# Kernel tuning notes

Measured on AMD Instinct MI355X. Metric: run time of the kernel, lower is better.

## Reference

```python
import jax, jax.numpy as jnp
import numpy as np

B, CD, NF, V, D = 16384, 13, 26, 100000, 64
BOT = [256, 128]
TOP = [512, 256, 128]
NUM_EMB = NF + 1            # 27 (bottom output + 26 categorical)
NUM_INTER = NUM_EMB * (NUM_EMB - 1) // 2  # 351
TOP_IN = NUM_INTER + NUM_EMB * D          # 2079
BN_INV = 1.0 / np.sqrt(1.0 + 1e-5)        # eval-mode BatchNorm: running_mean=0, running_var=1


def _lin(key, fan_in, fan_out):
    kw, kb = jax.random.split(key)
    s = 1.0 / np.sqrt(fan_in)
    W = jax.random.uniform(kw, (fan_in, fan_out), minval=-s, maxval=s, dtype=jnp.float32)
    b = jax.random.uniform(kb, (fan_out,), minval=-s, maxval=s, dtype=jnp.float32)
    return W, b


def setup_inputs() -> dict:
    key = jax.random.key(0)
    ks = jax.random.split(key, 16)
    continuous = jax.random.normal(ks[0], (B, CD), dtype=jnp.float32)
    cat_idx = jax.random.randint(ks[1], (B, NF), 0, V, dtype=jnp.int32)
    emb_tables = jax.random.normal(ks[2], (NF, V, D), dtype=jnp.float32)  # nn.Embedding init ~ N(0,1)
    W1, b1 = _lin(ks[3], CD, BOT[0]);   g1 = jnp.ones((BOT[0],)); be1 = jnp.zeros((BOT[0],))
    W2, b2 = _lin(ks[4], BOT[0], BOT[1]); g2 = jnp.ones((BOT[1],)); be2 = jnp.zeros((BOT[1],))
    W3, b3 = _lin(ks[5], BOT[1], D)
    W4, b4 = _lin(ks[6], TOP_IN, TOP[0]); g4 = jnp.ones((TOP[0],)); be4 = jnp.zeros((TOP[0],))
    W5, b5 = _lin(ks[7], TOP[0], TOP[1]); g5 = jnp.ones((TOP[1],)); be5 = jnp.zeros((TOP[1],))
    W6, b6 = _lin(ks[8], TOP[1], TOP[2]); g6 = jnp.ones((TOP[2],)); be6 = jnp.zeros((TOP[2],))
    W7, b7 = _lin(ks[9], TOP[2], 1)
    return dict(continuous=continuous, cat_idx=cat_idx, emb_tables=emb_tables,
                W1=W1, b1=b1, g1=g1, be1=be1, W2=W2, b2=b2, g2=g2, be2=be2, W3=W3, b3=b3,
                W4=W4, b4=b4, g4=g4, be4=be4, W5=W5, b5=b5, g5=g5, be5=be5,
                W6=W6, b6=b6, g6=g6, be6=be6, W7=W7, b7=b7)


def _bn(x, g, b):
    # eval-mode BatchNorm1d with running_mean=0, running_var=1
    return g * (x * BN_INV) + b


def reference(continuous, cat_idx, emb_tables,
              W1, b1, g1, be1, W2, b2, g2, be2, W3, b3,
              W4, b4, g4, be4, W5, b5, g5, be5, W6, b6, g6, be6, W7, b7):
    # Bottom MLP: 13 -> 256 -> 128 -> 64
    h = jax.nn.relu(_bn(continuous @ W1 + b1, g1, be1))
    h = jax.nn.relu(_bn(h @ W2 + b2, g2, be2))
    bottom = h @ W3 + b3                         # [B, D]

    # Embedding gather: one table per categorical feature
    emb = emb_tables[jnp.arange(NF), cat_idx]    # [B, NF, D]
    all_emb = jnp.concatenate([bottom[:, None, :], emb], axis=1)  # [B, 27, D]

    # Pairwise dot-product interactions via one bmm + triu gather
    Z = jnp.einsum('bnd,bmd->bnm', all_emb, all_emb)              # [B, 27, 27]
    iu, ju = np.triu_indices(NUM_EMB, k=1)                        # row-major i<j (matches torch loop order)
    inter = Z[:, iu, ju]                                          # [B, 351]

    top_in = jnp.concatenate([inter, all_emb.reshape(all_emb.shape[0], -1)], axis=1)  # [B, 2079]

    # Top MLP: 2079 -> 512 -> 256 -> 128 -> 1
    t = jax.nn.relu(_bn(top_in @ W4 + b4, g4, be4))
    t = jax.nn.relu(_bn(t @ W5 + b5, g5, be5))
    t = jax.nn.relu(_bn(t @ W6 + b6, g6, be6))
    scores = t @ W7 + b7                                          # [B, 1]
    return scores
```

## Files before the change

kernel.cpp:

```cpp
#include <hip/hip_runtime.h>
#include <stdint.h>
#include <stddef.h>

#define BATCH   16384
#define CDIM    13
#define NFEAT   26
#define VROWS   100000
#define EDIM    64
#define NEMB    27
#define NINTER  351
#define TOPIN   2079
#define KP4     2112
#define BN_INVF 0.9999950000374997f

typedef __attribute__((ext_vector_type(8)))  __bf16 bf16x8;
typedef __attribute__((ext_vector_type(4)))  float  f32x4;
typedef __attribute__((ext_vector_type(16))) float  f32x16;
typedef __attribute__((ext_vector_type(4)))  uint32_t uint4v;

__device__ __forceinline__ uint32_t f2bf(float f){
  uint32_t u = __float_as_uint(f);
  return (u + 0x7fffu + ((u >> 16) & 1u)) >> 16;
}
__device__ __forceinline__ float bf2f(uint32_t h){ return __uint_as_float(h << 16); }
__device__ __forceinline__ uint32_t pack2(float a, float b){
  return f2bf(a) | (f2bf(b) << 16);
}
__device__ __forceinline__ void async_load16(const void* g, void* l){
  __builtin_amdgcn_global_load_lds(
      (const __attribute__((address_space(1))) uint32_t*)g,
      (__attribute__((address_space(3))) uint32_t*)l, 16, 0, 0);
}
__device__ __forceinline__ int rswz(int row){ return ((row ^ (row >> 3)) & 7) << 3; }

__device__ __forceinline__ void transpose_tile(
    float (*tile)[65], const float* __restrict__ src, unsigned short* __restrict__ dst,
    int K, int N, int Kpad, int remap, int kb, int nb){
  int k0 = kb*64, n0 = nb*64, t = threadIdx.x;
  int srcBase = remap ? ((k0 < 1728) ? (k0 + 351) : (k0 - 1728)) : k0;
  #pragma unroll 4
  for(int p = 0; p < 16; p++){
    int kr = p*4 + (t >> 6), nc = t & 63;
    float v = 0.f;
    if(k0 + kr < K && (n0 + nc) < N) v = src[(size_t)(srcBase + kr) * N + n0 + nc];
    tile[kr][nc] = v;
  }
  __syncthreads();
  #pragma unroll 4
  for(int p = 0; p < 16; p++){
    int nr = p*4 + (t >> 6), kc = t & 63;
    if(k0 + kc < Kpad && (n0 + nr) < N)
      dst[(size_t)(n0 + nr) * Kpad + k0 + kc] = (unsigned short)f2bf(tile[kc][nr]);
  }
}

__global__ __launch_bounds__(256) void prep(
    const float* __restrict__ cont,
    const float* __restrict__ W1, const float* __restrict__ W2, const float* __restrict__ W3,
    const float* __restrict__ W4, const float* __restrict__ W5, const float* __restrict__ W6,
    unsigned short* __restrict__ xphi, unsigned short* __restrict__ xplo,
    unsigned short* __restrict__ W1t, unsigned short* __restrict__ W2t,
    unsigned short* __restrict__ W3t, unsigned short* __restrict__ W4t,
    unsigned short* __restrict__ W5t, unsigned short* __restrict__ W6t){
  __shared__ float tile[64][65];
  int bid = blockIdx.x;
  if(bid < 264){ transpose_tile(tile, W4, W4t, TOPIN, 512, KP4, 1, bid % 33, bid / 33); }
  else if(bid < 296){ int r = bid-264; transpose_tile(tile, W5, W5t, 512, 256, 512, 0, r % 8, r / 8); }
  else if(bid < 304){ int r = bid-296; transpose_tile(tile, W6, W6t, 256, 128, 256, 0, r % 4, r / 4); }
  else if(bid < 312){ int r = bid-304; transpose_tile(tile, W2, W2t, 256, 128, 256, 0, r % 4, r / 4); }
  else if(bid < 314){ int r = bid-312; transpose_tile(tile, W3, W3t, 128, 64, 128, 0, r, 0); }
  else if(bid < 318){ int r = bid-314; transpose_tile(tile, W1, W1t, CDIM, 256, 32, 0, 0, r); }
  else {
    int row = (bid - 318) * 256 + threadIdx.x;
    const float* xr = cont + (size_t)row * CDIM;
    uint32_t uh[16], ul[16];
    #pragma unroll
    for(int k = 0; k < 16; k++){
      uint32_t h0=0, h1=0, l0=0, l1=0;
      if(2*k < CDIM){
        float x = xr[2*k]; h0 = f2bf(x); l0 = f2bf(x - bf2f(h0));
      }
      if(2*k+1 < CDIM){
        float x = xr[2*k+1]; h1 = f2bf(x); l1 = f2bf(x - bf2f(h1));
      }
      uh[k] = h0 | (h1 << 16);
      ul[k] = l0 | (l1 << 16);
    }
    #pragma unroll
    for(int s = 0; s < 4; s++){
      uint4v vh, vl;
      #pragma unroll
      for(int e = 0; e < 4; e++){ vh[e] = uh[4*s+e]; vl[e] = ul[4*s+e]; }
      *(uint4v*)(xphi + (size_t)row*32 + s*8) = vh;
      *(uint4v*)(xplo + (size_t)row*32 + s*8) = vl;
    }
  }
}

__global__ __launch_bounds__(256) void bottom_mfma(
    const unsigned short* __restrict__ xphi, const unsigned short* __restrict__ xplo,
    const unsigned short* __restrict__ W1t, const unsigned short* __restrict__ W2t,
    const unsigned short* __restrict__ W3t,
    const float* __restrict__ b1, const float* __restrict__ g1, const float* __restrict__ be1,
    const float* __restrict__ b2, const float* __restrict__ g2, const float* __restrict__ be2,
    const float* __restrict__ b3,
    unsigned short* __restrict__ bottomBF){
  __shared__ unsigned short h1hi[64*256];
  __shared__ unsigned short h1lo[64*256];
  __shared__ unsigned short h2hi[64*128];
  __shared__ unsigned short h2lo[64*128];
  int t = threadIdx.x, w = t >> 6, l = t & 63;
  int m0 = blockIdx.x * 64;
  int lr = l & 15, lk = (l >> 4) * 8;

  {
    bf16x8 axh[4], axl[4];
    #pragma unroll
    for(int mt = 0; mt < 4; mt++){
      size_t ro = (size_t)(m0 + mt*16 + lr) * 32 + lk;
      axh[mt] = *(const bf16x8*)(xphi + ro);
      axl[mt] = *(const bf16x8*)(xplo + ro);
    }
    #pragma unroll
    for(int nt = 0; nt < 4; nt++){
      int n = (w*4 + nt)*16 + lr;
      bf16x8 bw = *(const bf16x8*)(W1t + (size_t)n*32 + lk);
      f32x4 acc[4];
      #pragma unroll
      for(int mt = 0; mt < 4; mt++){
        #pragma unroll
        for(int e = 0; e < 4; e++) acc[mt][e] = 0.f;
        acc[mt] = __builtin_amdgcn_mfma_f32_16x16x32_bf16(axh[mt], bw, acc[mt], 0, 0, 0);
        acc[mt] = __builtin_amdgcn_mfma_f32_16x16x32_bf16(axl[mt], bw, acc[mt], 0, 0, 0);
      }
      float sc = g1[n]*BN_INVF, bo = be1[n], bi = b1[n];
      #pragma unroll
      for(int mt = 0; mt < 4; mt++){
        #pragma unroll
        for(int q = 0; q < 4; q++){
          int row = mt*16 + (l >> 4)*4 + q;
          float y = fmaxf(sc*(acc[mt][q] + bi) + bo, 0.f);
          uint32_t hb = f2bf(y);
          int idx = row*256 + (n ^ rswz(row));
          h1hi[idx] = (unsigned short)hb;
          h1lo[idx] = (unsigned short)f2bf(y - bf2f(hb));
        }
      }
    }
  }
  __syncthreads();

  {
    f32x4 acc[4][2];
    #pragma unroll
    for(int mt = 0; mt < 4; mt++)
      #pragma unroll
      for(int nt = 0; nt < 2; nt++)
        #pragma unroll
        for(int e = 0; e < 4; e++) acc[mt][nt][e] = 0.f;
    for(int ks = 0; ks < 8; ks++){
      bf16x8 bw[2];
      #pragma unroll
      for(int nt = 0; nt < 2; nt++){
        int n = (w*2 + nt)*16 + lr;
        bw[nt] = *(const bf16x8*)(W2t + (size_t)n*256 + ks*32 + lk);
      }
      #pragma unroll
      for(int mt = 0; mt < 4; mt++){
        int row = mt*16 + lr;
        int idx = row*256 + ((ks*32 + lk) ^ rswz(row));
        bf16x8 ah = *(const bf16x8*)(h1hi + idx);
        bf16x8 al = *(const bf16x8*)(h1lo + idx);
        #pragma unroll
        for(int nt = 0; nt < 2; nt++){
          acc[mt][nt] = __builtin_amdgcn_mfma_f32_16x16x32_bf16(ah, bw[nt], acc[mt][nt], 0, 0, 0);
          acc[mt][nt] = __builtin_amdgcn_mfma_f32_16x16x32_bf16(al, bw[nt], acc[mt][nt], 0, 0, 0);
        }
      }
    }
    #pragma unroll
    for(int nt = 0; nt < 2; nt++){
      int n = (w*2 + nt)*16 + lr;
      float sc = g2[n]*BN_INVF, bo = be2[n], bi = b2[n];
      #pragma unroll
      for(int mt = 0; mt < 4; mt++){
        #pragma unroll
        for(int q = 0; q < 4; q++){
          int row = mt*16 + (l >> 4)*4 + q;
          float y = fmaxf(sc*(acc[mt][nt][q] + bi) + bo, 0.f);
          uint32_t hb = f2bf(y);
          int idx = row*128 + (n ^ rswz(row));
          h2hi[idx] = (unsigned short)hb;
          h2lo[idx] = (unsigned short)f2bf(y - bf2f(hb));
        }
      }
    }
  }
  __syncthreads();

  {
    f32x4 acc[4];
    #pragma unroll
    for(int mt = 0; mt < 4; mt++)
      #pragma unroll
      for(int e = 0; e < 4; e++) acc[mt][e] = 0.f;
    int n = w*16 + lr;
    for(int ks = 0; ks < 4; ks++){
      bf16x8 bw = *(const bf16x8*)(W3t + (size_t)n*128 + ks*32 + lk);
      #pragma unroll
      for(int mt = 0; mt < 4; mt++){
        int row = mt*16 + lr;
        int idx = row*128 + ((ks*32 + lk) ^ rswz(row));
        bf16x8 ah = *(const bf16x8*)(h2hi + idx);
        bf16x8 al = *(const bf16x8*)(h2lo + idx);
        acc[mt] = __builtin_amdgcn_mfma_f32_16x16x32_bf16(ah, bw, acc[mt], 0, 0, 0);
        acc[mt] = __builtin_amdgcn_mfma_f32_16x16x32_bf16(al, bw, acc[mt], 0, 0, 0);
      }
    }
    float bi = b3[n];
    #pragma unroll
    for(int mt = 0; mt < 4; mt++){
      #pragma unroll
      for(int q = 0; q < 4; q++){
        int row = m0 + mt*16 + (l >> 4)*4 + q;
        bottomBF[(size_t)row*64 + n] = (unsigned short)f2bf(acc[mt][q] + bi);
      }
    }
  }
}

__global__ __launch_bounds__(256) void interact(
    const unsigned short* __restrict__ bottomBF, const int* __restrict__ cat_idx,
    const float* __restrict__ emb, unsigned short* __restrict__ top_in){
  __shared__ unsigned short inter_s[4][352];
  int w = threadIdx.x >> 6, l = threadIdx.x & 63;
  int b = blockIdx.x * 4 + w;
  int r = l & 31, h = l >> 5;
  bool active = (r < NEMB);
  uint4v q[4];
  if(active && r == 0){
    const unsigned short* sb = bottomBF + (size_t)b * 64;
    #pragma unroll
    for(int s = 0; s < 4; s++) q[s] = *(const uint4v*)(sb + h*8 + s*16);
  } else if(active){
    int f = r - 1;
    int idx = cat_idx[b * NFEAT + f];
    const float* src = emb + ((size_t)f * VROWS + (size_t)idx) * 64;
    #pragma unroll
    for(int s = 0; s < 4; s++){
      int k0 = h*8 + s*16;
      float4 v0 = *(const float4*)(src + k0);
      float4 v1 = *(const float4*)(src + k0 + 4);
      q[s][0] = pack2(v0.x, v0.y); q[s][1] = pack2(v0.z, v0.w);
      q[s][2] = pack2(v1.x, v1.y); q[s][3] = pack2(v1.z, v1.w);
    }
  } else {
    #pragma unroll
    for(int s = 0; s < 4; s++){ q[s][0]=0; q[s][1]=0; q[s][2]=0; q[s][3]=0; }
  }
  if(active){
    #pragma unroll
    for(int s = 0; s < 4; s++)
      *(uint4v*)(top_in + (size_t)b*KP4 + r*64 + h*8 + s*16) = q[s];
  }
  f32x16 acc;
  #pragma unroll
  for(int i = 0; i < 16; i++) acc[i] = 0.f;
  #pragma unroll
  for(int s = 0; s < 4; s++){
    bf16x8 a = __builtin_bit_cast(bf16x8, q[s]);
    acc = __builtin_amdgcn_mfma_f32_32x32x16_bf16(a, a, acc, 0, 0, 0);
  }
  if(active){
    #pragma unroll
    for(int qq = 0; qq < 16; qq++){
      int i = (qq & 3) + 8*(qq >> 2) + 4*h;
      if(i < r){
        int p = i*(53 - i)/2 + (r - i - 1);
        inter_s[w][p] = (unsigned short)f2bf(acc[qq]);
      }
    }
  }
  __syncthreads();
  size_t basei = (size_t)b*KP4 + 1728;
  for(int t0 = l; t0 < 176; t0 += 64){
    uint32_t lo = inter_s[w][2*t0];
    uint32_t hi = (2*t0 + 1 < NINTER) ? (uint32_t)inter_s[w][2*t0 + 1] : 0u;
    *(uint32_t*)(top_in + basei + 2*t0) = lo | (hi << 16);
  }
  if(l < 16) *(uint32_t*)(top_in + (size_t)b*KP4 + 2080 + 2*l) = 0;
}

template<int KSTEPS, int NB>
__global__ __launch_bounds__(512, 2) void gemm_deep(
    const unsigned short* __restrict__ A, int sA,
    const unsigned short* __restrict__ Bw, int sB,
    const float* __restrict__ bias, const float* __restrict__ gg,
    const float* __restrict__ be,
    unsigned short* __restrict__ out, int sOut){
  __shared__ char smem[3*49152];
  int nwg = gridDim.x;
  int bid = blockIdx.x;
  int lin = (bid & 7) * (nwg >> 3) + (bid >> 3);
  int m0 = (lin / NB) * 256, n0 = (lin % NB) * 128;
  int t = threadIdx.x, w = t >> 6, l = t & 63;
  int wr = (w >> 1) * 64, wc = (w & 1) * 64;
  f32x4 acc[4][4];
  #pragma unroll
  for(int i = 0; i < 4; i++)
    #pragma unroll
    for(int j = 0; j < 4; j++)
      #pragma unroll
      for(int e = 0; e < 4; e++) acc[i][j][e] = 0.f;

  const unsigned short* g[6];
  int ldsOff[6];
  #pragma unroll
  for(int i = 0; i < 6; i++){
    if(i < 4){
      int o = i*8192 + t*16;
      int row = o >> 7;
      int cb  = (o & 127) ^ ((row & 7) << 4);
      g[i] = A + (size_t)(m0 + row)*sA + (cb >> 1);
      ldsOff[i] = o;
    } else {
      int o = (i-4)*8192 + t*16;
      int row = o >> 7;
      int cb  = (o & 127) ^ ((row & 7) << 4);
      g[i] = Bw + (size_t)(n0 + row)*sB + (cb >> 1);
      ldsOff[i] = 32768 + o;
    }
  }
  int lr = l & 15;
  int o1 = ((l >> 4) * 16) ^ ((l & 7) << 4);

  #pragma unroll
  for(int i = 0; i < 6; i++) async_load16(g[i], smem + ldsOff[i]);
  #pragma unroll
  for(int i = 0; i < 6; i++) async_load16(g[i] + 64, smem + 49152 + ldsOff[i]);
  asm volatile("s_waitcnt vmcnt(6)" ::: "memory");
  __builtin_amdgcn_s_barrier();

  for(int kt = 0; kt < KSTEPS; kt++){
    int cur = kt % 3;
    int nxt2 = (kt + 2) % 3;
    int ksrc = (kt + 2 < KSTEPS) ? (kt + 2) : (KSTEPS - 1);
    const char* bA = smem + cur*49152;
    const char* bB = bA + 32768;
    #pragma unroll
    for(int i = 0; i < 3; i++)
      async_load16(g[i] + ksrc*64, smem + nxt2*49152 + ldsOff[i]);
    {
      bf16x8 af[4], bfr[4];
      #pragma unroll
      for(int x = 0; x < 4; x++){
        af[x]  = *(const bf16x8*)(bA + (wr + x*16 + lr)*128 + o1);
        bfr[x] = *(const bf16x8*)(bB + (wc + x*16 + lr)*128 + o1);
      }
      __builtin_amdgcn_s_barrier();
      __builtin_amdgcn_s_setprio(1);
      #pragma unroll
      for(int tr = 0; tr < 4; tr++)
        #pragma unroll
        for(int tc = 0; tc < 4; tc++)
          acc[tr][tc] = __builtin_amdgcn_mfma_f32_16x16x32_bf16(af[tr], bfr[tc], acc[tr][tc], 0, 0, 0);
      __builtin_amdgcn_s_setprio(0);
    }
    __builtin_amdgcn_s_barrier();
    #pragma unroll
    for(int i = 3; i < 6; i++)
      async_load16(g[i] + ksrc*64, smem + nxt2*49152 + ldsOff[i]);
    {
      bf16x8 af[4], bfr[4];
      int ko = o1 ^ 64;
      #pragma unroll
      for(int x = 0; x < 4; x++){
        af[x]  = *(const bf16x8*)(bA + (wr + x*16 + lr)*128 + ko);
        bfr[x] = *(const bf16x8*)(bB + (wc + x*16 + lr)*128 + ko);
      }
      asm volatile("s_waitcnt vmcnt(6)" ::: "memory");
      __builtin_amdgcn_s_barrier();
      __builtin_amdgcn_s_setprio(1);
      #pragma unroll
      for(int tr = 0; tr < 4; tr++)
        #pragma unroll
        for(int tc = 0; tc < 4; tc++)
          acc[tr][tc] = __builtin_amdgcn_mfma_f32_16x16x32_bf16(af[tr], bfr[tc], acc[tr][tc], 0, 0, 0);
      __builtin_amdgcn_s_setprio(0);
    }
    __builtin_amdgcn_s_barrier();
  }

  #pragma unroll
  for(int tc = 0; tc < 4; tc++){
    int n = n0 + wc + tc*16 + lr;
    float sc = gg[n]*BN_INVF, bo = be[n], bi = bias[n];
    #pragma unroll
    for(int tr = 0; tr < 4; tr++){
      int mb = m0 + wr + tr*16 + (l >> 4)*4;
      #pragma unroll
      for(int qq = 0; qq < 4; qq++){
        float y = fmaxf(sc*(acc[tr][tc][qq] + bi) + bo, 0.f);
        out[(size_t)(mb + qq)*sOut + n] = (unsigned short)f2bf(y);
      }
    }
  }
}

__global__ __launch_bounds__(256) void gemm_tail(
    const unsigned short* __restrict__ h4,
    const unsigned short* __restrict__ W5t,
    const float* __restrict__ b5, const float* __restrict__ g5, const float* __restrict__ be5,
    const unsigned short* __restrict__ W6t,
    const float* __restrict__ b6, const float* __restrict__ g6, const float* __restrict__ be6,
    const float* __restrict__ W7, const float* __restrict__ b7,
    float* __restrict__ scores){
  __shared__ char smem[74752];
  unsigned short* h5 = (unsigned short*)(smem + 40960);
  float* pscore = (float*)(smem + 73728);
  int t = threadIdx.x, w = t >> 6, l = t & 63;
  int m0 = blockIdx.x * 64;
  int lr = l & 15;
  int o1 = ((l >> 4) * 16) ^ ((l & 7) << 4);

  f32x4 acc5[4][4];
  #pragma unroll
  for(int i = 0; i < 4; i++)
    #pragma unroll
    for(int j = 0; j < 4; j++)
      #pragma unroll
      for(int e = 0; e < 4; e++) acc5[i][j][e] = 0.f;

  const unsigned short* gA[2]; int ldsA[2];
  #pragma unroll
  for(int i = 0; i < 2; i++){
    int o = i*4096 + t*16;
    int row = o >> 7;
    int cb = (o & 127) ^ ((row & 7) << 4);
    gA[i] = h4 + (size_t)(m0 + row)*512 + (cb >> 1);
    ldsA[i] = o;
  }
  const unsigned short* gB[8]; int ldsB[8];
  #pragma unroll
  for(int i = 0; i < 8; i++){
    int o = i*4096 + t*16;
    int row = o >> 7;
    int cb = (o & 127) ^ ((row & 7) << 4);
    gB[i] = W5t + (size_t)row*512 + (cb >> 1);
    ldsB[i] = 8192 + o;
  }

  for(int kt = 0; kt < 8; kt++){
    #pragma unroll
    for(int i = 0; i < 2; i++) async_load16(gA[i] + kt*64, smem + ldsA[i]);
    #pragma unroll
    for(int i = 0; i < 8; i++) async_load16(gB[i] + kt*64, smem + ldsB[i]);
    __syncthreads();
    #pragma unroll
    for(int ks = 0; ks < 2; ks++){
      int ko = o1 ^ (ks << 6);
      bf16x8 af[4], bfr[4];
      #pragma unroll
      for(int x = 0; x < 4; x++){
        af[x]  = *(const bf16x8*)(smem + (x*16 + lr)*128 + ko);
        bfr[x] = *(const bf16x8*)(smem + 8192 + (w*64 + x*16 + lr)*128 + ko);
      }
      #pragma unroll
      for(int tr = 0; tr < 4; tr++)
        #pragma unroll
        for(int tc = 0; tc < 4; tc++)
          acc5[tr][tc] = __builtin_amdgcn_mfma_f32_16x16x32_bf16(af[tr], bfr[tc], acc5[tr][tc], 0, 0, 0);
    }
    __syncthreads();
  }

  #pragma unroll
  for(int i = 0; i < 8; i++){
    int o = i*4096 + t*16;
    int row = o >> 8;
    int cb = (o & 255) ^ ((row & 15) << 4);
    async_load16(W6t + (size_t)row*256 + (cb >> 1), smem + o);
  }
  #pragma unroll
  for(int tc = 0; tc < 4; tc++){
    int c = w*64 + tc*16 + lr;
    float sc = g5[c]*BN_INVF, bo = be5[c], bi = b5[c];
    #pragma unroll
    for(int tr = 0; tr < 4; tr++){
      #pragma unroll
      for(int qq = 0; qq < 4; qq++){
        int row = tr*16 + (l >> 4)*4 + qq;
        float y = fmaxf(sc*(acc5[tr][tc][qq] + bi) + bo, 0.f);
        h5[row*256 + (c ^ rswz(row))] = (unsigned short)f2bf(y);
      }
    }
  }
  __syncthreads();

  f32x4 acc6[4][2];
  #pragma unroll
  for(int i = 0; i < 4; i++)
    #pragma unroll
    for(int j = 0; j < 2; j++)
      #pragma unroll
      for(int e = 0; e < 4; e++) acc6[i][j][e] = 0.f;
  int lk = (l >> 4) * 8;
  int lk2 = (l >> 4) * 16;
  #pragma unroll
  for(int half = 0; half < 2; half++){
    if(half == 1){
      __syncthreads();
      #pragma unroll
      for(int i = 0; i < 8; i++){
        int o = i*4096 + t*16;
        int row = o >> 8;
        int cb = (o & 255) ^ ((row & 15) << 4);
        async_load16(W6t + (size_t)row*256 + 128 + (cb >> 1), smem + o);
      }
      __syncthreads();
    }
    #pragma unroll
    for(int ks = 0; ks < 4; ks++){
      bf16x8 af6[4], bfr6[2];
      #pragma unroll
      for(int mt = 0; mt < 4; mt++){
        int row = mt*16 + lr;
        af6[mt] = *(const bf16x8*)(h5 + row*256 + ((half*128 + ks*32 + lk) ^ rswz(row)));
      }
      #pragma unroll
      for(int nt = 0; nt < 2; nt++){
        int row = w*32 + nt*16 + lr;
        bfr6[nt] = *(const bf16x8*)(smem + row*256 + ((ks*64 + lk2) ^ (lr << 4)));
      }
      #pragma unroll
      for(int mt = 0; mt < 4; mt++)
        #pragma unroll
        for(int nt = 0; nt < 2; nt++)
          acc6[mt][nt] = __builtin_amdgcn_mfma_f32_16x16x32_bf16(af6[mt], bfr6[nt], acc6[mt][nt], 0, 0, 0);
    }
  }

  float pr[16];
  #pragma unroll
  for(int nt = 0; nt < 2; nt++){
    int c = w*32 + nt*16 + lr;
    float sc = g6[c]*BN_INVF, bo = be6[c], bi = b6[c];
    float w7c = W7[c];
    #pragma unroll
    for(int mt = 0; mt < 4; mt++){
      #pragma unroll
      for(int qq = 0; qq < 4; qq++){
        float v = fmaxf(sc*(acc6[mt][nt][qq] + bi) + bo, 0.f) * w7c;
        if(nt == 0) pr[mt*4 + qq] = v; else pr[mt*4 + qq] += v;
      }
    }
  }
  #pragma unroll
  for(int mask = 1; mask < 16; mask <<= 1){
    #pragma unroll
    for(int i = 0; i < 16; i++) pr[i] += __shfl_xor(pr[i], mask, 64);
  }
  if(lr == 0){
    #pragma unroll
    for(int mt = 0; mt < 4; mt++)
      #pragma unroll
      for(int qq = 0; qq < 4; qq++)
        pscore[w*64 + mt*16 + (l >> 4)*4 + qq] = pr[mt*4 + qq];
  }
  __syncthreads();
  if(t < 64){
    float s = b7[0] + pscore[t] + pscore[64 + t] + pscore[128 + t] + pscore[192 + t];
    scores[m0 + t] = s;
  }
}

static inline size_t alignup(size_t x){ return (x + 255) & ~(size_t)255; }

extern "C" void kernel_launch(void* const* d_in, const int* in_sizes, int n_in,
                              void* d_out, int out_size, void* d_ws, size_t ws_size,
                              hipStream_t stream){
  const float* cont = (const float*)d_in[0];
  const int*   cat  = (const int*)  d_in[1];
  const float* emb  = (const float*)d_in[2];
  const float* W1 = (const float*)d_in[3],  *b1 = (const float*)d_in[4];
  const float* g1 = (const float*)d_in[5],  *be1= (const float*)d_in[6];
  const float* W2 = (const float*)d_in[7],  *b2 = (const float*)d_in[8];
  const float* g2 = (const float*)d_in[9],  *be2= (const float*)d_in[10];
  const float* W3 = (const float*)d_in[11], *b3 = (const float*)d_in[12];
  const float* W4 = (const float*)d_in[13], *b4 = (const float*)d_in[14];
  const float* g4 = (const float*)d_in[15], *be4= (const float*)d_in[16];
  const float* W5 = (const float*)d_in[17], *b5 = (const float*)d_in[18];
  const float* g5 = (const float*)d_in[19], *be5= (const float*)d_in[20];
  const float* W6 = (const float*)d_in[21], *b6 = (const float*)d_in[22];
  const float* g6 = (const float*)d_in[23], *be6= (const float*)d_in[24];
  const float* W7 = (const float*)d_in[25], *b7 = (const float*)d_in[26];

  char* ws = (char*)d_ws;
  unsigned short* bottomBF = (unsigned short*)ws; ws += alignup((size_t)BATCH*64*2);
  unsigned short* xphi = (unsigned short*)ws; ws += alignup((size_t)BATCH*32*2);
  unsigned short* xplo = (unsigned short*)ws; ws += alignup((size_t)BATCH*32*2);
  unsigned short* W1t  = (unsigned short*)ws; ws += alignup((size_t)256*32*2);
  unsigned short* W2t  = (unsigned short*)ws; ws += alignup((size_t)128*256*2);
  unsigned short* W3t  = (unsigned short*)ws; ws += alignup((size_t)64*128*2);
  unsigned short* topi = (unsigned short*)ws; ws += alignup((size_t)BATCH*KP4*2);
  unsigned short* W4t  = (unsigned short*)ws; ws += alignup((size_t)512*KP4*2);
  unsigned short* W5t  = (unsigned short*)ws; ws += alignup((size_t)256*512*2);
  unsigned short* W6t  = (unsigned short*)ws; ws += alignup((size_t)128*256*2);
  unsigned short* h4   = (unsigned short*)ws; ws += alignup((size_t)BATCH*512*2);
  (void)ws_size; (void)n_in; (void)in_sizes; (void)out_size;

  hipLaunchKernelGGL(prep, dim3(382), dim3(256), 0, stream,
                     cont, W1, W2, W3, W4, W5, W6,
                     xphi, xplo, W1t, W2t, W3t, W4t, W5t, W6t);
  hipLaunchKernelGGL(bottom_mfma, dim3(BATCH/64), dim3(256), 0, stream,
                     xphi, xplo, W1t, W2t, W3t,
                     b1, g1, be1, b2, g2, be2, b3, bottomBF);
  hipLaunchKernelGGL(interact, dim3(BATCH/4), dim3(256), 0, stream, bottomBF, cat, emb, topi);
  hipLaunchKernelGGL((gemm_deep<33, 4>), dim3(256), dim3(512), 0, stream,
                     topi, KP4, W4t, KP4, b4, g4, be4, h4, 512);
  hipLaunchKernelGGL(gemm_tail, dim3(256), dim3(256), 0, stream,
                     h4, W5t, b5, g5, be5, W6t, b6, g6, be6, W7, b7, (float*)d_out);
}
```

Before: 115.9 us.

## Fuse bottom MLP with interaction kernel and use 32x32 MFMA in deep GEMM

```diff
diff --git a/kernel.cpp b/kernel.cpp
--- a/kernel.cpp
+++ b/kernel.cpp
@@ -55,10 +55,8 @@
 }
 
 __global__ __launch_bounds__(256) void prep(
-    const float* __restrict__ cont,
     const float* __restrict__ W1, const float* __restrict__ W2, const float* __restrict__ W3,
     const float* __restrict__ W4, const float* __restrict__ W5, const float* __restrict__ W6,
-    unsigned short* __restrict__ xphi, unsigned short* __restrict__ xplo,
     unsigned short* __restrict__ W1t, unsigned short* __restrict__ W2t,
     unsigned short* __restrict__ W3t, unsigned short* __restrict__ W4t,
     unsigned short* __restrict__ W5t, unsigned short* __restrict__ W6t){
@@ -69,226 +67,196 @@
   else if(bid < 304){ int r = bid-296; transpose_tile(tile, W6, W6t, 256, 128, 256, 0, r % 4, r / 4); }
   else if(bid < 312){ int r = bid-304; transpose_tile(tile, W2, W2t, 256, 128, 256, 0, r % 4, r / 4); }
   else if(bid < 314){ int r = bid-312; transpose_tile(tile, W3, W3t, 128, 64, 128, 0, r, 0); }
-  else if(bid < 318){ int r = bid-314; transpose_tile(tile, W1, W1t, CDIM, 256, 32, 0, 0, r); }
-  else {
-    int row = (bid - 318) * 256 + threadIdx.x;
-    const float* xr = cont + (size_t)row * CDIM;
-    uint32_t uh[16], ul[16];
-    #pragma unroll
-    for(int k = 0; k < 16; k++){
-      uint32_t h0=0, h1=0, l0=0, l1=0;
-      if(2*k < CDIM){
-        float x = xr[2*k]; h0 = f2bf(x); l0 = f2bf(x - bf2f(h0));
-      }
-      if(2*k+1 < CDIM){
-        float x = xr[2*k+1]; h1 = f2bf(x); l1 = f2bf(x - bf2f(h1));
-      }
-      uh[k] = h0 | (h1 << 16);
-      ul[k] = l0 | (l1 << 16);
-    }
-    #pragma unroll
-    for(int s = 0; s < 4; s++){
-      uint4v vh, vl;
-      #pragma unroll
-      for(int e = 0; e < 4; e++){ vh[e] = uh[4*s+e]; vl[e] = ul[4*s+e]; }
-      *(uint4v*)(xphi + (size_t)row*32 + s*8) = vh;
-      *(uint4v*)(xplo + (size_t)row*32 + s*8) = vl;
-    }
-  }
-}
-
-__global__ __launch_bounds__(256) void bottom_mfma(
-    const unsigned short* __restrict__ xphi, const unsigned short* __restrict__ xplo,
+  else               { int r = bid-314; transpose_tile(tile, W1, W1t, CDIM, 256, 32, 0, 0, r); }
+}
+
+__global__ __launch_bounds__(256) void bottom_interact(
+    const float* __restrict__ cont, const int* __restrict__ cat_idx,
+    const float* __restrict__ emb,
     const unsigned short* __restrict__ W1t, const unsigned short* __restrict__ W2t,
     const unsigned short* __restrict__ W3t,
     const float* __restrict__ b1, const float* __restrict__ g1, const float* __restrict__ be1,
     const float* __restrict__ b2, const float* __restrict__ g2, const float* __restrict__ be2,
     const float* __restrict__ b3,
-    unsigned short* __restrict__ bottomBF){
-  __shared__ unsigned short h1hi[64*256];
-  __shared__ unsigned short h1lo[64*256];
-  __shared__ unsigned short h2hi[64*128];
-  __shared__ unsigned short h2lo[64*128];
+    unsigned short* __restrict__ top_in){
+  __shared__ unsigned short h1hi[16*256];
+  __shared__ unsigned short h1lo[16*256];
+  __shared__ unsigned short h2hi[16*128];
+  __shared__ unsigned short h2lo[16*128];
+  __shared__ unsigned short bot_s[16*64];
+  __shared__ unsigned short inter_s[16][352];
   int t = threadIdx.x, w = t >> 6, l = t & 63;
-  int m0 = blockIdx.x * 64;
-  int lr = l & 15, lk = (l >> 4) * 8;
-
+  int m0 = blockIdx.x * 16;
+  int lr = l & 15, lg = l >> 4, lk = lg * 8;
+  int r = l & 31, h = l >> 5;
+  bool activeB = (r >= 1 && r < NEMB);
+
+  int idx4[4];
+  #pragma unroll
+  for(int s = 0; s < 4; s++){
+    int b = m0 + w*4 + s;
+    idx4[s] = activeB ? cat_idx[b*NFEAT + (r-1)] : 0;
+  }
+
+  bf16x8 axh, axl;
   {
-    bf16x8 axh[4], axl[4];
-    #pragma unroll
-    for(int mt = 0; mt < 4; mt++){
-      size_t ro = (size_t)(m0 + mt*16 + lr) * 32 + lk;
-      axh[mt] = *(const bf16x8*)(xphi + ro);
-      axl[mt] = *(const bf16x8*)(xplo + ro);
-    }
+    uint32_t uh[4], ul[4];
+    #pragma unroll
+    for(int p = 0; p < 4; p++){
+      float x0 = 0.f, x1 = 0.f;
+      int k0 = lk + 2*p;
+      if(k0 < CDIM)     x0 = cont[(size_t)(m0 + lr)*CDIM + k0];
+      if(k0 + 1 < CDIM) x1 = cont[(size_t)(m0 + lr)*CDIM + k0 + 1];
+      uint32_t h0 = f2bf(x0), h1b = f2bf(x1);
+      uh[p] = h0 | (h1b << 16);
+      ul[p] = f2bf(x0 - bf2f(h0)) | (f2bf(x1 - bf2f(h1b)) << 16);
+    }
+    uint4v vh, vl;
+    #pragma unroll
+    for(int e = 0; e < 4; e++){ vh[e] = uh[e]; vl[e] = ul[e]; }
+    axh = __builtin_bit_cast(bf16x8, vh);
+    axl = __builtin_bit_cast(bf16x8, vl);
+  }
+
+  {
     #pragma unroll
     for(int nt = 0; nt < 4; nt++){
-      int n = (w*4 + nt)*16 + lr;
+      int n = w*64 + nt*16 + lr;
       bf16x8 bw = *(const bf16x8*)(W1t + (size_t)n*32 + lk);
-      f32x4 acc[4];
-      #pragma unroll
-      for(int mt = 0; mt < 4; mt++){
-        #pragma unroll
-        for(int e = 0; e < 4; e++) acc[mt][e] = 0.f;
-        acc[mt] = __builtin_amdgcn_mfma_f32_16x16x32_bf16(axh[mt], bw, acc[mt], 0, 0, 0);
-        acc[mt] = __builtin_amdgcn_mfma_f32_16x16x32_bf16(axl[mt], bw, acc[mt], 0, 0, 0);
-      }
+      f32x4 acc;
+      #pragma unroll
+      for(int e = 0; e < 4; e++) acc[e] = 0.f;
+      acc = __builtin_amdgcn_mfma_f32_16x16x32_bf16(axh, bw, acc, 0, 0, 0);
+      acc = __builtin_amdgcn_mfma_f32_16x16x32_bf16(axl, bw, acc, 0, 0, 0);
       float sc = g1[n]*BN_INVF, bo = be1[n], bi = b1[n];
       #pragma unroll
-      for(int mt = 0; mt < 4; mt++){
-        #pragma unroll
-        for(int q = 0; q < 4; q++){
-          int row = mt*16 + (l >> 4)*4 + q;
-          float y = fmaxf(sc*(acc[mt][q] + bi) + bo, 0.f);
-          uint32_t hb = f2bf(y);
-          int idx = row*256 + (n ^ rswz(row));
-          h1hi[idx] = (unsigned short)hb;
-          h1lo[idx] = (unsigned short)f2bf(y - bf2f(hb));
-        }
+      for(int q = 0; q < 4; q++){
+        int ro = lg*4 + q;
+        float y = fmaxf(sc*(acc[q] + bi) + bo, 0.f);
+        uint32_t hb = f2bf(y);
+        int idx = ro*256 + (n ^ rswz(ro));
+        h1hi[idx] = (unsigned short)hb;
+        h1lo[idx] = (unsigned short)f2bf(y - bf2f(hb));
       }
     }
   }
   __syncthreads();
 
   {
-    f32x4 acc[4][2];
-    #pragma unroll
-    for(int mt = 0; mt < 4; mt++)
-      #pragma unroll
-      for(int nt = 0; nt < 2; nt++)
-        #pragma unroll
-        for(int e = 0; e < 4; e++) acc[mt][nt][e] = 0.f;
+    f32x4 acc[2];
+    #pragma unroll
+    for(int nt = 0; nt < 2; nt++)
+      #pragma unroll
+      for(int e = 0; e < 4; e++) acc[nt][e] = 0.f;
     for(int ks = 0; ks < 8; ks++){
       bf16x8 bw[2];
       #pragma unroll
       for(int nt = 0; nt < 2; nt++){
-        int n = (w*2 + nt)*16 + lr;
+        int n = w*32 + nt*16 + lr;
         bw[nt] = *(const bf16x8*)(W2t + (size_t)n*256 + ks*32 + lk);
       }
-      #pragma unroll
-      for(int mt = 0; mt < 4; mt++){
-        int row = mt*16 + lr;
-        int idx = row*256 + ((ks*32 + lk) ^ rswz(row));
-        bf16x8 ah = *(const bf16x8*)(h1hi + idx);
-        bf16x8 al = *(const bf16x8*)(h1lo + idx);
-        #pragma unroll
-        for(int nt = 0; nt < 2; nt++){
-          acc[mt][nt] = __builtin_amdgcn_mfma_f32_16x16x32_bf16(ah, bw[nt], acc[mt][nt], 0, 0, 0);
-          acc[mt][nt] = __builtin_amdgcn_mfma_f32_16x16x32_bf16(al, bw[nt], acc[mt][nt], 0, 0, 0);
-        }
+      int ai = lr*256 + ((ks*32 + lk) ^ rswz(lr));
+      bf16x8 ah = *(const bf16x8*)(h1hi + ai);
+      bf16x8 al = *(const bf16x8*)(h1lo + ai);
+      #pragma unroll
+      for(int nt = 0; nt < 2; nt++){
+        acc[nt] = __builtin_amdgcn_mfma_f32_16x16x32_bf16(ah, bw[nt], acc[nt], 0, 0, 0);
+        acc[nt] = __builtin_amdgcn_mfma_f32_16x16x32_bf16(al, bw[nt], acc[nt], 0, 0, 0);
       }
     }
     #pragma unroll
     for(int nt = 0; nt < 2; nt++){
-      int n = (w*2 + nt)*16 + lr;
+      int n = w*32 + nt*16 + lr;
       float sc = g2[n]*BN_INVF, bo = be2[n], bi = b2[n];
       #pragma unroll
-      for(int mt = 0; mt < 4; mt++){
-        #pragma unroll
-        for(int q = 0; q < 4; q++){
-          int row = mt*16 + (l >> 4)*4 + q;
-          float y = fmaxf(sc*(acc[mt][nt][q] + bi) + bo, 0.f);
-          uint32_t hb = f2bf(y);
-          int idx = row*128 + (n ^ rswz(row));
-          h2hi[idx] = (unsigned short)hb;
-          h2lo[idx] = (unsigned short)f2bf(y - bf2f(hb));
-        }
+      for(int q = 0; q < 4; q++){
+        int ro = lg*4 + q;
+        float y = fmaxf(sc*(acc[nt][q] + bi) + bo, 0.f);
+        uint32_t hb = f2bf(y);
+        int idx = ro*128 + (n ^ rswz(ro));
+        h2hi[idx] = (unsigned short)hb;
+        h2lo[idx] = (unsigned short)f2bf(y - bf2f(hb));
       }
     }
   }
   __syncthreads();
 
   {
-    f32x4 acc[4];
-    #pragma unroll
-    for(int mt = 0; mt < 4; mt++)
-      #pragma unroll
-      for(int e = 0; e < 4; e++) acc[mt][e] = 0.f;
+    f32x4 acc;
+    #pragma unroll
+    for(int e = 0; e < 4; e++) acc[e] = 0.f;
     int n = w*16 + lr;
     for(int ks = 0; ks < 4; ks++){
       bf16x8 bw = *(const bf16x8*)(W3t + (size_t)n*128 + ks*32 + lk);
-      #pragma unroll
-      for(int mt = 0; mt < 4; mt++){
-        int row = mt*16 + lr;
-        int idx = row*128 + ((ks*32 + lk) ^ rswz(row));
-        bf16x8 ah = *(const bf16x8*)(h2hi + idx);
-        bf16x8 al = *(const bf16x8*)(h2lo + idx);
-        acc[mt] = __builtin_amdgcn_mfma_f32_16x16x32_bf16(ah, bw, acc[mt], 0, 0, 0);
-        acc[mt] = __builtin_amdgcn_mfma_f32_16x16x32_bf16(al, bw, acc[mt], 0, 0, 0);
-      }
+      int ai = lr*128 + ((ks*32 + lk) ^ rswz(lr));
+      bf16x8 ah = *(const bf16x8*)(h2hi + ai);
+      bf16x8 al = *(const bf16x8*)(h2lo + ai);
+      acc = __builtin_amdgcn_mfma_f32_16x16x32_bf16(ah, bw, acc, 0, 0, 0);
+      acc = __builtin_amdgcn_mfma_f32_16x16x32_bf16(al, bw, acc, 0, 0, 0);
     }
     float bi = b3[n];
     #pragma unroll
-    for(int mt = 0; mt < 4; mt++){
-      #pragma unroll
-      for(int q = 0; q < 4; q++){
-        int row = m0 + mt*16 + (l >> 4)*4 + q;
-        bottomBF[(size_t)row*64 + n] = (unsigned short)f2bf(acc[mt][q] + bi);
-      }
-    }
-  }
-}
-
-__global__ __launch_bounds__(256) void interact(
-    const unsigned short* __restrict__ bottomBF, const int* __restrict__ cat_idx,
-    const float* __restrict__ emb, unsigned short* __restrict__ top_in){
-  __shared__ unsigned short inter_s[4][352];
-  int w = threadIdx.x >> 6, l = threadIdx.x & 63;
-  int b = blockIdx.x * 4 + w;
-  int r = l & 31, h = l >> 5;
-  bool active = (r < NEMB);
-  uint4v q[4];
-  if(active && r == 0){
-    const unsigned short* sb = bottomBF + (size_t)b * 64;
-    #pragma unroll
-    for(int s = 0; s < 4; s++) q[s] = *(const uint4v*)(sb + h*8 + s*16);
-  } else if(active){
-    int f = r - 1;
-    int idx = cat_idx[b * NFEAT + f];
-    const float* src = emb + ((size_t)f * VROWS + (size_t)idx) * 64;
-    #pragma unroll
-    for(int s = 0; s < 4; s++){
-      int k0 = h*8 + s*16;
-      float4 v0 = *(const float4*)(src + k0);
-      float4 v1 = *(const float4*)(src + k0 + 4);
-      q[s][0] = pack2(v0.x, v0.y); q[s][1] = pack2(v0.z, v0.w);
-      q[s][2] = pack2(v1.x, v1.y); q[s][3] = pack2(v1.z, v1.w);
-    }
-  } else {
-    #pragma unroll
-    for(int s = 0; s < 4; s++){ q[s][0]=0; q[s][1]=0; q[s][2]=0; q[s][3]=0; }
-  }
-  if(active){
-    #pragma unroll
-    for(int s = 0; s < 4; s++)
-      *(uint4v*)(top_in + (size_t)b*KP4 + r*64 + h*8 + s*16) = q[s];
-  }
-  f32x16 acc;
-  #pragma unroll
-  for(int i = 0; i < 16; i++) acc[i] = 0.f;
-  #pragma unroll
+    for(int q = 0; q < 4; q++){
+      int ro = lg*4 + q;
+      bot_s[ro*64 + n] = (unsigned short)f2bf(acc[q] + bi);
+    }
+  }
+  __syncthreads();
+
   for(int s = 0; s < 4; s++){
-    bf16x8 a = __builtin_bit_cast(bf16x8, q[s]);
-    acc = __builtin_amdgcn_mfma_f32_32x32x16_bf16(a, a, acc, 0, 0, 0);
-  }
-  if(active){
-    #pragma unroll
-    for(int qq = 0; qq < 16; qq++){
-      int i = (qq & 3) + 8*(qq >> 2) + 4*h;
-      if(i < r){
-        int p = i*(53 - i)/2 + (r - i - 1);
-        inter_s[w][p] = (unsigned short)f2bf(acc[qq]);
-      }
-    }
-  }
-  __syncthreads();
-  size_t basei = (size_t)b*KP4 + 1728;
-  for(int t0 = l; t0 < 176; t0 += 64){
-    uint32_t lo = inter_s[w][2*t0];
-    uint32_t hi = (2*t0 + 1 < NINTER) ? (uint32_t)inter_s[w][2*t0 + 1] : 0u;
-    *(uint32_t*)(top_in + basei + 2*t0) = lo | (hi << 16);
-  }
-  if(l < 16) *(uint32_t*)(top_in + (size_t)b*KP4 + 2080 + 2*l) = 0;
+    int sb = w*4 + s;
+    int b = m0 + sb;
+    uint4v q[4];
+    if(r == 0){
+      #pragma unroll
+      for(int p = 0; p < 4; p++)
+        q[p] = *(const uint4v*)(bot_s + sb*64 + h*8 + p*16);
+    } else if(activeB){
+      const float* src = emb + ((size_t)(r-1)*VROWS + (size_t)idx4[s])*64;
+      #pragma unroll
+      for(int p = 0; p < 4; p++){
+        int k0 = h*8 + p*16;
+        float4 v0 = *(const float4*)(src + k0);
+        float4 v1 = *(const float4*)(src + k0 + 4);
+        q[p][0] = pack2(v0.x, v0.y); q[p][1] = pack2(v0.z, v0.w);
+        q[p][2] = pack2(v1.x, v1.y); q[p][3] = pack2(v1.z, v1.w);
+      }
+    } else {
+      #pragma unroll
+      for(int p = 0; p < 4; p++){ q[p][0]=0; q[p][1]=0; q[p][2]=0; q[p][3]=0; }
+    }
+    if(r < NEMB){
+      #pragma unroll
+      for(int p = 0; p < 4; p++)
+        *(uint4v*)(top_in + (size_t)b*KP4 + r*64 + h*8 + p*16) = q[p];
+    }
+    f32x16 acc;
+    #pragma unroll
+    for(int i = 0; i < 16; i++) acc[i] = 0.f;
+    #pragma unroll
+    for(int p = 0; p < 4; p++){
+      bf16x8 a = __builtin_bit_cast(bf16x8, q[p]);
+      acc = __builtin_amdgcn_mfma_f32_32x32x16_bf16(a, a, acc, 0, 0, 0);
+    }
+    if(r < NEMB){
+      #pragma unroll
+      for(int qq = 0; qq < 16; qq++){
+        int i = (qq & 3) + 8*(qq >> 2) + 4*h;
+        if(i < r){
+          int p = i*(53 - i)/2 + (r - i - 1);
+          inter_s[sb][p] = (unsigned short)f2bf(acc[qq]);
+        }
+      }
+    }
+    asm volatile("s_waitcnt lgkmcnt(0)" ::: "memory");
+    size_t basei = (size_t)b*KP4 + 1728;
+    for(int t0 = l; t0 < 176; t0 += 64){
+      uint32_t lo = inter_s[sb][2*t0];
+      uint32_t hi = (2*t0 + 1 < NINTER) ? (uint32_t)inter_s[sb][2*t0 + 1] : 0u;
+      *(uint32_t*)(top_in + basei + 2*t0) = lo | (hi << 16);
+    }
+    if(l < 16) *(uint32_t*)(top_in + (size_t)b*KP4 + 2080 + 2*l) = 0;
+  }
 }
 
 template<int KSTEPS, int NB>
@@ -305,13 +273,14 @@
   int m0 = (lin / NB) * 256, n0 = (lin % NB) * 128;
   int t = threadIdx.x, w = t >> 6, l = t & 63;
   int wr = (w >> 1) * 64, wc = (w & 1) * 64;
-  f32x4 acc[4][4];
-  #pragma unroll
-  for(int i = 0; i < 4; i++)
-    #pragma unroll
-    for(int j = 0; j < 4; j++)
-      #pragma unroll
-      for(int e = 0; e < 4; e++) acc[i][j][e] = 0.f;
+  int l31 = l & 31, l5 = l >> 5;
+  f32x16 acc[2][2];
+  #pragma unroll
+  for(int i = 0; i < 2; i++)
+    #pragma unroll
+    for(int j = 0; j < 2; j++)
+      #pragma unroll
+      for(int e = 0; e < 16; e++) acc[i][j][e] = 0.f;
 
   const unsigned short* g[6];
   int ldsOff[6];
@@ -331,8 +300,7 @@
       ldsOff[i] = 32768 + o;
     }
   }
-  int lr = l & 15;
-  int o1 = ((l >> 4) * 16) ^ ((l & 7) << 4);
+  int swz = (l31 & 7) << 4;
 
   #pragma unroll
   for(int i = 0; i < 6; i++) async_load16(g[i], smem + ldsOff[i]);
@@ -348,60 +316,54 @@
     const char* bA = smem + cur*49152;
     const char* bB = bA + 32768;
     #pragma unroll
-    for(int i = 0; i < 3; i++)
-      async_load16(g[i] + ksrc*64, smem + nxt2*49152 + ldsOff[i]);
-    {
-      bf16x8 af[4], bfr[4];
-      #pragma unroll
-      for(int x = 0; x < 4; x++){
-        af[x]  = *(const bf16x8*)(bA + (wr + x*16 + lr)*128 + o1);
-        bfr[x] = *(const bf16x8*)(bB + (wc + x*16 + lr)*128 + o1);
-      }
+    for(int ph = 0; ph < 2; ph++){
+      if(ph == 0){
+        #pragma unroll
+        for(int i = 0; i < 3; i++)
+          async_load16(g[i] + ksrc*64, smem + nxt2*49152 + ldsOff[i]);
+      } else {
+        #pragma unroll
+        for(int i = 3; i < 6; i++)
+          async_load16(g[i] + ksrc*64, smem + nxt2*49152 + ldsOff[i]);
+      }
+      bf16x8 af[2][2], bfr[2][2];
+      #pragma unroll
+      for(int ks = 0; ks < 2; ks++){
+        int ko = ((ph*2 + ks)*32 + l5*16) ^ swz;
+        #pragma unroll
+        for(int mt = 0; mt < 2; mt++)
+          af[ks][mt]  = *(const bf16x8*)(bA + (wr + mt*32 + l31)*128 + ko);
+        #pragma unroll
+        for(int nt = 0; nt < 2; nt++)
+          bfr[ks][nt] = *(const bf16x8*)(bB + (wc + nt*32 + l31)*128 + ko);
+      }
+      if(ph == 1) asm volatile("s_waitcnt vmcnt(6)" ::: "memory");
       __builtin_amdgcn_s_barrier();
       __builtin_amdgcn_s_setprio(1);
       #pragma unroll
-      for(int tr = 0; tr < 4; tr++)
-        #pragma unroll
-        for(int tc = 0; tc < 4; tc++)
-          acc[tr][tc] = __builtin_amdgcn_mfma_f32_16x16x32_bf16(af[tr], bfr[tc], acc[tr][tc], 0, 0, 0);
+      for(int ks = 0; ks < 2; ks++)
+        #pragma unroll
+        for(int mt = 0; mt < 2; mt++)
+          #pragma unroll
+          for(int nt = 0; nt < 2; nt++)
+            acc[mt][nt] = __builtin_amdgcn_mfma_f32_32x32x16_bf16(af[ks][mt], bfr[ks][nt], acc[mt][nt], 0, 0, 0);
       __builtin_amdgcn_s_setprio(0);
-    }
-    __builtin_amdgcn_s_barrier();
-    #pragma unroll
-    for(int i = 3; i < 6; i++)
-      async_load16(g[i] + ksrc*64, smem + nxt2*49152 + ldsOff[i]);
-    {
-      bf16x8 af[4], bfr[4];
-      int ko = o1 ^ 64;
-      #pragma unroll
-      for(int x = 0; x < 4; x++){
-        af[x]  = *(const bf16x8*)(bA + (wr + x*16 + lr)*128 + ko);
-        bfr[x] = *(const bf16x8*)(bB + (wc + x*16 + lr)*128 + ko);
-      }
-      asm volatile("s_waitcnt vmcnt(6)" ::: "memory");
       __builtin_amdgcn_s_barrier();
-      __builtin_amdgcn_s_setprio(1);
-      #pragma unroll
-      for(int tr = 0; tr < 4; tr++)
-        #pragma unroll
-        for(int tc = 0; tc < 4; tc++)
-          acc[tr][tc] = __builtin_amdgcn_mfma_f32_16x16x32_bf16(af[tr], bfr[tc], acc[tr][tc], 0, 0, 0);
-      __builtin_amdgcn_s_setprio(0);
-    }
-    __builtin_amdgcn_s_barrier();
-  }
-
-  #pragma unroll
-  for(int tc = 0; tc < 4; tc++){
-    int n = n0 + wc + tc*16 + lr;
-    float sc = gg[n]*BN_INVF, bo = be[n], bi = bias[n];
-    #pragma unroll
-    for(int tr = 0; tr < 4; tr++){
-      int mb = m0 + wr + tr*16 + (l >> 4)*4;
-      #pragma unroll
-      for(int qq = 0; qq < 4; qq++){
-        float y = fmaxf(sc*(acc[tr][tc][qq] + bi) + bo, 0.f);
-        out[(size_t)(mb + qq)*sOut + n] = (unsigned short)f2bf(y);
+    }
+  }
+
+  #pragma unroll
+  for(int mt = 0; mt < 2; mt++){
+    #pragma unroll
+    for(int nt = 0; nt < 2; nt++){
+      int col = n0 + wc + nt*32 + l31;
+      float sc = gg[col]*BN_INVF, bo = be[col], bi = bias[col];
+      #pragma unroll
+      for(int reg = 0; reg < 16; reg++){
+        int rowf = (reg & 3) + 8*(reg >> 2) + 4*l5;
+        int row = m0 + wr + mt*32 + rowf;
+        float y = fmaxf(sc*(acc[mt][nt][reg] + bi) + bo, 0.f);
+        out[(size_t)row*sOut + col] = (unsigned short)f2bf(y);
       }
     }
   }
@@ -596,9 +558,6 @@
   const float* W7 = (const float*)d_in[25], *b7 = (const float*)d_in[26];
 
   char* ws = (char*)d_ws;
-  unsigned short* bottomBF = (unsigned short*)ws; ws += alignup((size_t)BATCH*64*2);
-  unsigned short* xphi = (unsigned short*)ws; ws += alignup((size_t)BATCH*32*2);
-  unsigned short* xplo = (unsigned short*)ws; ws += alignup((size_t)BATCH*32*2);
   unsigned short* W1t  = (unsigned short*)ws; ws += alignup((size_t)256*32*2);
   unsigned short* W2t  = (unsigned short*)ws; ws += alignup((size_t)128*256*2);
   unsigned short* W3t  = (unsigned short*)ws; ws += alignup((size_t)64*128*2);
@@ -609,13 +568,12 @@
   unsigned short* h4   = (unsigned short*)ws; ws += alignup((size_t)BATCH*512*2);
   (void)ws_size; (void)n_in; (void)in_sizes; (void)out_size;
 
-  hipLaunchKernelGGL(prep, dim3(382), dim3(256), 0, stream,
-                     cont, W1, W2, W3, W4, W5, W6,
-                     xphi, xplo, W1t, W2t, W3t, W4t, W5t, W6t);
-  hipLaunchKernelGGL(bottom_mfma, dim3(BATCH/64), dim3(256), 0, stream,
-                     xphi, xplo, W1t, W2t, W3t,
-                     b1, g1, be1, b2, g2, be2, b3, bottomBF);
-  hipLaunchKernelGGL(interact, dim3(BATCH/4), dim3(256), 0, stream, bottomBF, cat, emb, topi);
+  hipLaunchKernelGGL(prep, dim3(318), dim3(256), 0, stream,
+                     W1, W2, W3, W4, W5, W6,
+                     W1t, W2t, W3t, W4t, W5t, W6t);
+  hipLaunchKernelGGL(bottom_interact, dim3(BATCH/16), dim3(256), 0, stream,
+                     cont, cat, emb, W1t, W2t, W3t,
+                     b1, g1, be1, b2, g2, be2, b3, topi);
   hipLaunchKernelGGL((gemm_deep<33, 4>), dim3(256), dim3(512), 0, stream,
                      topi, KP4, W4t, KP4, b4, g4, be4, h4, 512);
   hipLaunchKernelGGL(gemm_tail, dim3(256), dim3(256), 0, stream,
```

Result: slower. 119.1 us (+2.7%).
